# Kernel optimization log

Hardware: AMD Instinct MI355X
Metric: run time of the kernel (lower is better)

The kernel has to match this reference:

```python
import jax, jax.numpy as jnp
import numpy as np

C_CURV = 0.1            # curvature k
SC = float(np.sqrt(C_CURV))
EPS = 1e-7


def _mobius_add(x, y, c):
    x2 = jnp.sum(x * x, -1, keepdims=True)
    y2 = jnp.sum(y * y, -1, keepdims=True)
    xy = jnp.sum(x * y, -1, keepdims=True)
    num = (1 + 2 * c * xy + c * y2) * x + (1 - c * x2) * y
    den = 1 + 2 * c * xy + c * c * x2 * y2
    return num / jnp.maximum(den, 1e-12)


def _mobius_scalarmul(r, x, c):
    sc = jnp.sqrt(c)
    n = jnp.linalg.norm(x, axis=-1, keepdims=True)
    t = jnp.clip(sc * n, EPS, 1.0 - 1e-6)
    return jnp.tanh(r * jnp.arctanh(t)) * x / jnp.maximum(sc * n, EPS)


def setup_inputs() -> dict:
    key = jax.random.key(0)
    k0, k1, k2, k3, k4 = jax.random.split(key, 5)
    B, N, V, D, NC = 64, 1024, 50257, 128, 10
    token_ids = jax.random.randint(k0, (B, N), 0, V)
    mask = jax.random.randint(k1, (B, N), 0, 2).astype(bool)
    emb = (jax.random.normal(k2, (V, D), jnp.float32) * 0.02).at[0].set(0.0)  # pad_id=0 row zeroed
    Wo = jax.random.normal(k3, (D, D + 1), jnp.float32) / np.sqrt(D + 1)
    bo = jnp.zeros((D,), jnp.float32)
    Wf = jax.random.normal(k4, (NC, D), jnp.float32) / np.sqrt(D)
    bf = jnp.zeros((NC,), jnp.float32)
    return {"token_ids": token_ids, "mask": mask, "emb": emb, "Wo": Wo, "bo": bo, "Wf": Wf, "bf": bf}


def reference(token_ids, mask, emb, Wo, bo, Wf, bf):
    c, sc = C_CURV, SC
    D = emb.shape[1]
    # embedding lookup (tangent vectors at origin)
    v = emb[token_ids]                                            # (B,N,D)
    # Lorentz expmap0 -> hyperboloid points in D+1
    nv = jnp.maximum(jnp.linalg.norm(v, axis=-1, keepdims=True), EPS)
    x = jnp.concatenate([jnp.cosh(sc * nv) / sc,
                         jnp.sinh(sc * nv) * v / (sc * nv)], -1)  # (B,N,D+1)
    # single-head attention, scores = -<xi,xj>_L (Lorentz inner), masked softmax
    sgn = jnp.concatenate([-jnp.ones((1,)), jnp.ones((D,))]).astype(x.dtype)
    scores = -jnp.einsum('bid,bjd->bij', x * sgn, x) / np.sqrt(D + 1)
    scores = jnp.where(mask[:, None, :], scores, -1e9)
    w = jax.nn.softmax(scores, axis=-1)
    # riemannian value aggregation: Lorentz centroid (weighted sum renormalized to hyperboloid)
    mu = jnp.einsum('bij,bjd->bid', w, x)
    inner = jnp.einsum('bid,d,bid->bi', mu, sgn, mu)
    mu = mu / (sc * jnp.sqrt(jnp.maximum(-inner, EPS))[..., None])
    # output projection (D+1 -> D) then Poincare expmap0 so points lie in the ball
    u = jnp.einsum('bid,od->bio', mu, Wo) + bo                    # (B,N,D)
    nu = jnp.maximum(jnp.linalg.norm(u, axis=-1, keepdims=True), EPS)
    y = jnp.tanh(sc * nu) * u / (sc * nu)                         # (B,N,D) in ball
    # sequential masked Mobius pooling: left-fold mobius_add over valid tokens, then scalarmul 1/n
    def step(acc, xm):
        xi, mi = xm                                               # (B,D), (B,)
        new = _mobius_add(acc, xi, c)
        return jnp.where(mi[:, None], new, acc), None
    acc0 = jnp.zeros_like(y[:, 0, :])
    acc, _ = jax.lax.scan(step, acc0, (jnp.swapaxes(y, 0, 1), jnp.swapaxes(mask, 0, 1)))
    cnt = jnp.sum(mask, axis=1)
    r = (1.0 / jnp.maximum(cnt, 1))[:, None].astype(y.dtype)
    pooled = _mobius_scalarmul(r, acc, c)
    pooled = jnp.where((cnt > 0)[:, None], pooled, y[:, 0, :])    # empty rows fall back to first token
    # LorentzMLR head: logmap0 then linear
    npn = jnp.maximum(jnp.linalg.norm(pooled, axis=-1, keepdims=True), EPS)
    t = jnp.clip(sc * npn, EPS, 1.0 - 1e-6)
    vlog = jnp.arctanh(t) * pooled / (sc * npn)
    return vlog @ Wf.T + bf                                       # (B, num_classes)
```

## Files before the change

### kernel.cpp

```cpp
#include <hip/hip_runtime.h>
#include <math.h>

#define B_    64
#define N_    1024
#define D_    128
#define DP1   129
#define NC_   10
#define QB    128
#define KT    32
#define SCf   0.31622776601683794f
#define SCALE 0.08804509063256238f

typedef __bf16 bf16x8 __attribute__((ext_vector_type(8)));
typedef float  f32x16 __attribute__((ext_vector_type(16)));
typedef unsigned long long ull;

#define MFMA(a, b, c) __builtin_amdgcn_mfma_f32_32x32x16_bf16((a), (b), (c), 0, 0, 0)

static __device__ __forceinline__ float dpp_add_step(float f, int ctrl, int rmask) {
    if (ctrl == 0x111) { int t = __builtin_amdgcn_update_dpp(0, __builtin_bit_cast(int, f), 0x111, 0xf, 0xf, true); return f + __builtin_bit_cast(float, t); }
    if (ctrl == 0x112) { int t = __builtin_amdgcn_update_dpp(0, __builtin_bit_cast(int, f), 0x112, 0xf, 0xf, true); return f + __builtin_bit_cast(float, t); }
    if (ctrl == 0x114) { int t = __builtin_amdgcn_update_dpp(0, __builtin_bit_cast(int, f), 0x114, 0xf, 0xf, true); return f + __builtin_bit_cast(float, t); }
    if (ctrl == 0x118) { int t = __builtin_amdgcn_update_dpp(0, __builtin_bit_cast(int, f), 0x118, 0xf, 0xf, true); return f + __builtin_bit_cast(float, t); }
    if (ctrl == 0x142 && rmask == 0xa) { int t = __builtin_amdgcn_update_dpp(0, __builtin_bit_cast(int, f), 0x142, 0xa, 0xf, true); return f + __builtin_bit_cast(float, t); }
    { int t = __builtin_amdgcn_update_dpp(0, __builtin_bit_cast(int, f), 0x143, 0xc, 0xf, true); return f + __builtin_bit_cast(float, t); }
}

static __device__ __forceinline__ float wave_sum64(float f) {
    f = dpp_add_step(f, 0x111, 0xf);
    f = dpp_add_step(f, 0x112, 0xf);
    f = dpp_add_step(f, 0x114, 0xf);
    f = dpp_add_step(f, 0x118, 0xf);
    f = dpp_add_step(f, 0x142, 0xa);
    f = dpp_add_step(f, 0x143, 0xc);
    return __builtin_bit_cast(float, __builtin_amdgcn_readlane(__builtin_bit_cast(int, f), 63));
}

static __device__ __forceinline__ float half_sum32(float f, int half) {
    f = dpp_add_step(f, 0x111, 0xf);
    f = dpp_add_step(f, 0x112, 0xf);
    f = dpp_add_step(f, 0x114, 0xf);
    f = dpp_add_step(f, 0x118, 0xf);
    f = dpp_add_step(f, 0x142, 0xa);
    float s0 = __builtin_bit_cast(float, __builtin_amdgcn_readlane(__builtin_bit_cast(int, f), 31));
    float s1 = __builtin_bit_cast(float, __builtin_amdgcn_readlane(__builtin_bit_cast(int, f), 63));
    return half ? s1 : s0;
}

static __device__ __forceinline__ float readlane_f(float v, int lane) {
    return __builtin_bit_cast(float, __builtin_amdgcn_readlane(__builtin_bit_cast(int, v), lane));
}

static __device__ __forceinline__ bf16x8 ld_lds8(const __bf16* p) {
    union { bf16x8 v; ull q[2]; } u;
    u.q[0] = *(const ull*)(p);
    u.q[1] = *(const ull*)(p + 4);
    return u.v;
}

__global__ __launch_bounds__(256) void k_detect_mask(const int* __restrict__ mask_w,
                                                     int* __restrict__ flag) {
    __shared__ int bad;
    if (threadIdx.x == 0) bad = 0;
    __syncthreads();
    int local = 0;
    for (int i = threadIdx.x; i < 16384; i += 256) {
        int v = mask_w[i];
        if (v != 0 && v != 1) local = 1;
    }
    if (local) atomicOr(&bad, 1);
    __syncthreads();
    if (threadIdx.x == 0) *flag = bad;
}

static __device__ __forceinline__ int read_mask(const int* mw, int is_i8, int idx) {
    if (is_i8) return (int)((const unsigned char*)mw)[idx];
    return mw[idx];
}

__global__ __launch_bounds__(256) void k_prep_wo(const float* __restrict__ Wo,
                                                 __bf16* __restrict__ Woh,
                                                 __bf16* __restrict__ Wol) {
    int idx = blockIdx.x * 256 + threadIdx.x;
    if (idx >= 128 * 144) return;
    int o = idx / 144, d = idx - o * 144;
    float v = (d < DP1) ? Wo[o * DP1 + d] : 0.f;
    __bf16 h = (__bf16)v;
    Woh[idx] = h;
    Wol[idx] = (__bf16)(v - (float)h);
}

__global__ __launch_bounds__(256) void k_prep(const int* __restrict__ tok,
                                              const float* __restrict__ emb,
                                              __bf16* __restrict__ Xh, __bf16* __restrict__ Xl,
                                              float* __restrict__ X0g, float* __restrict__ X128g) {
    __shared__ float Xf[64][132];
    const int t = threadIdx.x, w = t >> 6, l = t & 63;
    const int base = blockIdx.x * 64;
    for (int it = 0; it < 16; ++it) {
        const int tk = w * 16 + it;
        const int id = tok[base + tk];
        const float2 v = ((const float2*)(emb + (size_t)id * D_))[l];
        float s = wave_sum64(v.x * v.x + v.y * v.y);
        float nv = fmaxf(sqrtf(s), 1e-7f);
        float a = SCf * nv;
        float a2 = a * a;
        float shc, ch;
        if (a < 0.5f) {
            shc = 1.f + a2 * (1.f/6.f) * (1.f + a2 * (1.f/20.f) * (1.f + a2 * (1.f/42.f)));
            ch  = 1.f + a2 * 0.5f * (1.f + a2 * (1.f/12.f) * (1.f + a2 * (1.f/30.f)));
        } else {
            float ea = __expf(a), ei = 1.f / ea;
            ch = 0.5f * (ea + ei);
            shc = 0.5f * (ea - ei) / a;
        }
        Xf[tk][1 + 2 * l] = v.x * shc;
        Xf[tk][2 + 2 * l] = v.y * shc;
        if (l == 0) Xf[tk][0] = ch / SCf;
    }
    __syncthreads();
    const int tk2 = t >> 2, dg = (t & 3) * 32;
    for (int i = 0; i < 32; i += 8) {
        bf16x8 hv, lv;
        #pragma unroll
        for (int j = 0; j < 8; ++j) {
            float f = Xf[tk2][dg + i + j];
            __bf16 h = (__bf16)f;
            hv[j] = h;
            lv[j] = (__bf16)(f - (float)h);
        }
        *(bf16x8*)(Xh + (size_t)(base + tk2) * D_ + dg + i) = hv;
        *(bf16x8*)(Xl + (size_t)(base + tk2) * D_ + dg + i) = lv;
    }
    if (t < 64) {
        X0g[base + t]   = Xf[t][0];
        X128g[base + t] = Xf[t][D_];
    }
}

__global__ __launch_bounds__(256, 2) void k_attn(
        const __bf16* __restrict__ Xh, const __bf16* __restrict__ Xl,
        const float* __restrict__ X0g, const float* __restrict__ X128g,
        const int* __restrict__ mask, const int* __restrict__ mflag,
        const __bf16* __restrict__ Woh, const __bf16* __restrict__ Wol,
        const float* __restrict__ bo,
        float* __restrict__ Y, float* __restrict__ Y2) {
    extern __shared__ char smem[];
    __bf16* KB = (__bf16*)smem;
    __bf16* Pb = (__bf16*)(smem + 33792);
    __shared__ float K0s[2][KT];
    __shared__ float K128s[2][KT];
    __shared__ int   Ms[2][KT];

    const int b    = blockIdx.x;
    const int qb   = blockIdx.y * QB;
    const int t    = threadIdx.x;
    const int w    = t >> 6;
    const int l    = t & 63;
    const int l31  = l & 31;
    const int half = l >> 5;
    const int is8  = *mflag;

    const size_t qrow = (size_t)(b * N_ + qb + w * 32 + l31);
    bf16x8 qfh[8], qfl[8];
    #pragma unroll
    for (int ks = 0; ks < 8; ++ks) {
        qfh[ks] = *(const bf16x8*)(Xh + qrow * D_ + ks * 16 + half * 8);
        qfl[ks] = *(const bf16x8*)(Xl + qrow * D_ + ks * 16 + half * 8);
    }
    float q0[16], q128[16];
    #pragma unroll
    for (int r = 0; r < 16; ++r) {
        const int qr = (r & 3) + 8 * (r >> 2) + 4 * half;
        q0[r]   = X0g[b * N_ + qb + w * 32 + qr];
        q128[r] = X128g[b * N_ + qb + w * 32 + qr];
    }

    const int skey = t >> 3, sck = t & 7;
    bf16x8 svh0, svh1, svl0, svl1;
    float  sK0 = 0.f, sK128 = 0.f;
    int    sM = 0;
    auto ldg_tile = [&](int kt) {
        const size_t kr = (size_t)(b * N_ + kt * KT + skey);
        svh0 = *(const bf16x8*)(Xh + kr * D_ + sck * 16);
        svh1 = *(const bf16x8*)(Xh + kr * D_ + sck * 16 + 8);
        svl0 = *(const bf16x8*)(Xl + kr * D_ + sck * 16);
        svl1 = *(const bf16x8*)(Xl + kr * D_ + sck * 16 + 8);
        if (t < KT) {
            sK0   = X0g[b * N_ + kt * KT + t];
            sK128 = X128g[b * N_ + kt * KT + t];
            sM    = read_mask(mask, is8, b * N_ + kt * KT + t);
        }
    };
    auto st_tile = [&](int buf) {
        __bf16* KH = KB + buf * 8448;
        __bf16* KL = KH + 4224;
        union { bf16x8 v; ull q[2]; } u;
        u.v = svh0; *(ull*)(KH + skey * 132 + sck * 16)      = u.q[0]; *(ull*)(KH + skey * 132 + sck * 16 + 4)  = u.q[1];
        u.v = svh1; *(ull*)(KH + skey * 132 + sck * 16 + 8)  = u.q[0]; *(ull*)(KH + skey * 132 + sck * 16 + 12) = u.q[1];
        u.v = svl0; *(ull*)(KL + skey * 132 + sck * 16)      = u.q[0]; *(ull*)(KL + skey * 132 + sck * 16 + 4)  = u.q[1];
        u.v = svl1; *(ull*)(KL + skey * 132 + sck * 16 + 8)  = u.q[0]; *(ull*)(KL + skey * 132 + sck * 16 + 12) = u.q[1];
        if (t < KT) { K0s[buf][t] = sK0; K128s[buf][t] = sK128; Ms[buf][t] = sM; }
    };

    f32x16 accM[4] = {};
    float  mu128p[16] = {};

    ldg_tile(0);
    st_tile(0);

    for (int kt = 0; kt < N_ / KT; ++kt) {
        __syncthreads();
        const int cur = kt & 1;
        const int ktn = (kt < 31) ? kt + 1 : 31;
        ldg_tile(ktn);

        const __bf16* KH = KB + cur * 8448;
        const __bf16* KL = KH + 4224;

        f32x16 accS = {};
        #pragma unroll
        for (int ks = 0; ks < 8; ++ks) {
            bf16x8 bh = ld_lds8(KH + l31 * 132 + ks * 16 + half * 8);
            bf16x8 bl = ld_lds8(KL + l31 * 132 + ks * 16 + half * 8);
            accS = MFMA(qfh[ks], bh, accS);
            accS = MFMA(qfh[ks], bl, accS);
            accS = MFMA(qfl[ks], bh, accS);
        }
        const float k0v = K0s[cur][l31], k128v = K128s[cur][l31];
        const int   mv  = Ms[cur][l31];
        #pragma unroll
        for (int r = 0; r < 16; ++r) {
            float sc = (2.f * q0[r] * k0v - accS[r] - q128[r] * k128v) * SCALE;
            float e  = mv ? __expf(sc) : 0.f;
            mu128p[r] += e * k128v;
            __bf16 eh = (__bf16)e;
            __bf16 el = (__bf16)(e - (float)eh);
            const int qr = (r & 3) + 8 * (r >> 2) + 4 * half;
            Pb[(w * 2 + 0) * 1152 + qr * 36 + l31] = eh;
            Pb[(w * 2 + 1) * 1152 + qr * 36 + l31] = el;
        }

        #pragma unroll
        for (int ks = 0; ks < 2; ++ks) {
            bf16x8 ah = ld_lds8(Pb + (w * 2 + 0) * 1152 + l31 * 36 + ks * 16 + half * 8);
            bf16x8 al = ld_lds8(Pb + (w * 2 + 1) * 1152 + l31 * 36 + ks * 16 + half * 8);
            #pragma unroll
            for (int nt = 0; nt < 4; ++nt) {
                const int cmp = nt * 32 + l31;
                bf16x8 bh, bl;
                #pragma unroll
                for (int j = 0; j < 8; ++j) {
                    const int key = ks * 16 + half * 8 + j;
                    bh[j] = KH[key * 132 + cmp];
                    bl[j] = KL[key * 132 + cmp];
                }
                accM[nt] = MFMA(ah, bh, accM[nt]);
                accM[nt] = MFMA(ah, bl, accM[nt]);
                accM[nt] = MFMA(al, bh, accM[nt]);
            }
        }

        st_tile(cur ^ 1);
    }

    #pragma unroll
    for (int r = 0; r < 16; ++r) mu128p[r] = half_sum32(mu128p[r], half);
    float rno[16];
    #pragma unroll
    for (int r = 0; r < 16; ++r) {
        float p = 0.f;
        #pragma unroll
        for (int nt = 0; nt < 4; ++nt) p += accM[nt][r] * accM[nt][r];
        if (l31 == 0) p -= 2.f * accM[0][r] * accM[0][r];
        p = half_sum32(p, half);
        float negI = -(p + mu128p[r] * mu128p[r]);
        negI = fmaxf(negI, 1e-7f);
        rno[r] = 1.f / (SCf * sqrtf(negI));
    }
    #pragma unroll
    for (int nt = 0; nt < 4; ++nt)
        #pragma unroll
        for (int r = 0; r < 16; ++r) accM[nt][r] *= rno[r];
    #pragma unroll
    for (int r = 0; r < 16; ++r) mu128p[r] *= rno[r];

    __syncthreads();
    __bf16* MuA = (__bf16*)smem + w * (32 * 148);
    #pragma unroll
    for (int r = 0; r < 16; ++r) {
        const int qr = (r & 3) + 8 * (r >> 2) + 4 * half;
        #pragma unroll
        for (int nt = 0; nt < 4; ++nt)
            MuA[qr * 148 + nt * 32 + l31] = (__bf16)accM[nt][r];
        if (l31 == 0) MuA[qr * 148 + 128] = (__bf16)mu128p[r];
        if (l31 >= 1 && l31 <= 15) MuA[qr * 148 + 128 + l31] = (__bf16)0.f;
    }
    bf16x8 Ah[9];
    #pragma unroll
    for (int ks = 0; ks < 9; ++ks) Ah[ks] = ld_lds8(MuA + l31 * 148 + ks * 16 + half * 8);
    #pragma unroll
    for (int r = 0; r < 16; ++r) {
        const int qr = (r & 3) + 8 * (r >> 2) + 4 * half;
        #pragma unroll
        for (int nt = 0; nt < 4; ++nt) {
            float m = accM[nt][r];
            MuA[qr * 148 + nt * 32 + l31] = (__bf16)(m - (float)(__bf16)m);
        }
        if (l31 == 0) {
            float m = mu128p[r];
            MuA[qr * 148 + 128] = (__bf16)(m - (float)(__bf16)m);
        }
    }
    bf16x8 Al[9];
    #pragma unroll
    for (int ks = 0; ks < 9; ++ks) Al[ks] = ld_lds8(MuA + l31 * 148 + ks * 16 + half * 8);

    f32x16 accU[4] = {};
    #pragma unroll
    for (int ks = 0; ks < 9; ++ks) {
        #pragma unroll
        for (int nt = 0; nt < 4; ++nt) {
            bf16x8 bh = *(const bf16x8*)(Woh + (size_t)(nt * 32 + l31) * 144 + ks * 16 + half * 8);
            bf16x8 bl = *(const bf16x8*)(Wol + (size_t)(nt * 32 + l31) * 144 + ks * 16 + half * 8);
            accU[nt] = MFMA(Ah[ks], bh, accU[nt]);
            accU[nt] = MFMA(Ah[ks], bl, accU[nt]);
            accU[nt] = MFMA(Al[ks], bh, accU[nt]);
        }
    }

    float bov[4];
    #pragma unroll
    for (int nt = 0; nt < 4; ++nt) bov[nt] = bo[nt * 32 + l31];
    #pragma unroll
    for (int r = 0; r < 16; ++r) {
        float p = 0.f;
        #pragma unroll
        for (int nt = 0; nt < 4; ++nt) {
            float uv = accU[nt][r] + bov[nt];
            accU[nt][r] = uv;
            p += uv * uv;
        }
        float nn = half_sum32(p, half);
        float nu = fmaxf(sqrtf(nn), 1e-7f);
        float aa = SCf * nu;
        float cf = tanhf(aa) / aa;
        const int qr = (r & 3) + 8 * (r >> 2) + 4 * half;
        const size_t row = (size_t)(b * N_ + qb + w * 32 + qr);
        #pragma unroll
        for (int nt = 0; nt < 4; ++nt)
            Y[row * D_ + nt * 32 + l31] = accU[nt][r] * cf;
        if (l31 == 0) Y2[row] = nn * cf * cf;
    }
}

__global__ __launch_bounds__(256) void k_gram(const float* __restrict__ Y,
                                              float* __restrict__ G) {
    const int c = blockIdx.x, b = blockIdx.y;
    const int t = threadIdx.x, w = t >> 6, l = t & 63;
    const int l31 = l & 31, half = l >> 5;
    const int rt = w >> 1, ct = w & 1;
    const size_t base = (size_t)(b * N_ + c * 64);
    const float* Ar = Y + (base + rt * 32 + l31) * D_;
    const float* Br = Y + (base + ct * 32 + l31) * D_;
    f32x16 acc = {};
    #pragma unroll
    for (int ks = 0; ks < 8; ++ks) {
        const int c0 = ks * 16 + half * 8;
        float4 a0 = *(const float4*)(Ar + c0);
        float4 a1 = *(const float4*)(Ar + c0 + 4);
        float4 b0 = *(const float4*)(Br + c0);
        float4 b1 = *(const float4*)(Br + c0 + 4);
        float av[8] = {a0.x, a0.y, a0.z, a0.w, a1.x, a1.y, a1.z, a1.w};
        float bv[8] = {b0.x, b0.y, b0.z, b0.w, b1.x, b1.y, b1.z, b1.w};
        bf16x8 ah, al, bh, bl;
        #pragma unroll
        for (int j = 0; j < 8; ++j) {
            __bf16 h = (__bf16)av[j]; ah[j] = h; al[j] = (__bf16)(av[j] - (float)h);
            __bf16 g = (__bf16)bv[j]; bh[j] = g; bl[j] = (__bf16)(bv[j] - (float)g);
        }
        acc = MFMA(ah, bh, acc);
        acc = MFMA(ah, bl, acc);
        acc = MFMA(al, bh, acc);
    }
    float* Gb = G + ((size_t)(b * 16 + c) << 12);
    #pragma unroll
    for (int r = 0; r < 16; ++r) {
        const int row = rt * 32 + (r & 3) + 8 * (r >> 2) + 4 * half;
        Gb[row * 64 + ct * 32 + l31] = acc[r];
    }
}

__global__ __launch_bounds__(64, 1) void k_pool(const float* __restrict__ Y,
                                                const float* __restrict__ Y2,
                                                const float* __restrict__ G,
                                                const int* __restrict__ mask,
                                                const int* __restrict__ mflag,
                                                const float* __restrict__ Wf,
                                                const float* __restrict__ bf_,
                                                float* __restrict__ out) {
    __shared__ float  prt[64][65];
    __shared__ double vb[D_];
    const int b = blockIdx.x, l = threadIdx.x;
    const int is8 = *mflag;

    int cl = 0;
    for (int i = l; i < N_; i += 64) cl += read_mask(mask, is8, b * N_ + i);
    const int cntT = (int)(wave_sum64((float)cl) + 0.5f);

    const float2* __restrict__ Yp = (const float2*)(Y + (size_t)b * N_ * D_) + l;
    const float*  __restrict__ Gp = G + ((size_t)b << 16) + l;
    const float*  __restrict__ Pp = Y2 + b * N_;

    float  GA[64], GB[64];
    float  py2A, py2B;
    int    msA, msB;
    float2 yring[2][16];

    #pragma unroll
    for (int i = 0; i < 64; ++i) GA[i] = Gp[i * 64];
    py2A = Pp[l];
    msA  = read_mask(mask, is8, b * N_ + l);
    #pragma unroll
    for (int k = 0; k < 16; ++k) yring[0][k] = Yp[(size_t)k * 64];

    float U0 = 0.f, U1 = 0.f, g = 0.f, Dh = 1.f, P = 0.f;

    auto chunk = [&](int c, float (&Gc)[64], float (&Gn)[64],
                     float py2c, float& py2n, int msc, int& msn) {
        const int cn = (c < 15) ? c + 1 : 15;
        #pragma unroll
        for (int i = 0; i < 64; ++i) Gn[i] = Gp[cn * 4096 + i * 64];
        py2n = Pp[cn * 64 + l];
        msn  = read_mask(mask, is8, b * N_ + cn * 64 + l);

        #pragma unroll
        for (int q = 0; q < 4; ++q) {
            #pragma unroll
            for (int k = 0; k < 16; ++k) {
                int gs = c * 64 + (q + 1) * 16 + k;
                if (gs > N_ - 1) gs = N_ - 1;
                yring[(q + 1) & 1][k] = Yp[(size_t)gs * 64];
            }
            #pragma unroll
            for (int k = 0; k < 16; ++k) {
                const int ir = q * 16 + k;
                const float2 yv  = yring[q & 1][k];
                const float  Gv  = Gc[ir];
                const float  py2 = readlane_f(py2c, ir);
                const bool   m   = (__builtin_amdgcn_readlane(msc, ir) != 0);
                const float Dsq   = Dh * Dh;
                const float Bh    = fmaf(-0.1f, P, Dsq);
                const float Donep = Dh * fmaf(0.1f, py2, 1.f);
                const float tP    = (0.01f * py2) * P;
                const float puy  = readlane_f(g, ir);
                const float Ahat = fmaf(0.2f, puy, Donep);
                float dh = fmaf(Dh, fmaf(0.2f, puy, Dh), tP);
                dh = fmaxf(dh, 1e-12f * Dsq);
                const float Draw = m ? dh : Dh;
                const float Am   = m ? Ahat : 1.f;
                const float Bm   = m ? Bh   : 0.f;
                const float Pn   = fmaf(Am, fmaf(Am, P, (2.f * Bm) * puy), (Bm * Bm) * py2);
                if ((k & 3) == 3) {
                    const int e = ilogbf(Draw);
                    const float Aef = ldexpf(Am, -e);
                    const float Bef = ldexpf(Bm, -e);
                    Dh = ldexpf(Draw, -e);
                    P  = ldexpf(Pn, -2 * e);
                    g  = fmaf(Aef, g, Bef * Gv);
                    U0 = fmaf(Aef, U0, Bef * yv.x);
                    U1 = fmaf(Aef, U1, Bef * yv.y);
                } else {
                    Dh = Draw;
                    P  = Pn;
                    g  = fmaf(Am, g, Bm * Gv);
                    U0 = fmaf(Am, U0, Bm * yv.x);
                    U1 = fmaf(Am, U1, Bm * yv.y);
                }
            }
        }
        if (c < 15) {
            const int nb = (c + 1) * 64;
            #pragma unroll
            for (int k0 = 0; k0 < 64; k0 += 16) {
                float2 tmp[16];
                #pragma unroll
                for (int k = 0; k < 16; ++k) tmp[k] = Yp[(size_t)(nb + k0 + k) * 64];
                #pragma unroll
                for (int k = 0; k < 16; ++k)
                    prt[k0 + k][l] = fmaf(U0, tmp[k].x, U1 * tmp[k].y);
            }
            float s0 = 0.f, s1 = 0.f, s2 = 0.f, s3 = 0.f;
            #pragma unroll
            for (int p = 0; p < 64; p += 4) {
                s0 += prt[l][p];     s1 += prt[l][p + 1];
                s2 += prt[l][p + 2]; s3 += prt[l][p + 3];
            }
            g = (s0 + s1) + (s2 + s3);
        }
    };

    for (int cc = 0; cc < 8; ++cc) {
        chunk(2 * cc,     GA, GB, py2A, py2B, msA, msB);
        chunk(2 * cc + 1, GB, GA, py2B, py2A, msB, msA);
    }

    const double SCd = 0.31622776601683794;
    const double sD = 1.0 / (double)Dh;
    double a0 = sD * (double)U0, a1 = sD * (double)U1;
    double n2 = fmax((double)P * (sD * sD), 0.0);
    double n = sqrt(n2);
    double tt = SCd * n;
    tt = fmin(fmax(tt, 1e-7), 1.0 - 1e-6);
    int cm = cntT > 0 ? cntT : 1;
    float rf = (float)(1.0 / (double)cm);
    double r = (double)rf;
    double dv = fmax(SCd * n, 1e-7);
    double f = tanh(r * atanh(tt)) / dv;
    double p0 = a0 * f, p1 = a1 * f;
    double q2;
    if (cntT == 0) {
        float2 y0v = *(const float2*)(Y + (size_t)(b * N_) * D_ + 2 * l);
        p0 = y0v.x; p1 = y0v.y;
        q2 = (double)Y2[b * N_];
    } else {
        q2 = f * f * n2;
    }
    double npn = fmax(sqrt(q2), 1e-7);
    double t2 = fmin(fmax(SCd * npn, 1e-7), 1.0 - 1e-6);
    double f2 = atanh(t2) / (SCd * npn);
    vb[2 * l]     = p0 * f2;
    vb[2 * l + 1] = p1 * f2;
    __syncthreads();

    if (l < NC_) {
        double o = (double)bf_[l];
        for (int d = 0; d < D_; ++d) o += vb[d] * (double)Wf[l * D_ + d];
        out[b * NC_ + l] = (float)o;
    }
}

extern "C" void kernel_launch(void* const* d_in, const int* in_sizes, int n_in,
                              void* d_out, int out_size, void* d_ws, size_t ws_size,
                              hipStream_t stream) {
    const int*   tok  = (const int*)d_in[0];
    const int*   mask = (const int*)d_in[1];
    const float* emb  = (const float*)d_in[2];
    const float* Wo   = (const float*)d_in[3];
    const float* bo   = (const float*)d_in[4];
    const float* Wf   = (const float*)d_in[5];
    const float* bf_  = (const float*)d_in[6];
    float* out = (float*)d_out;

    char* wsb = (char*)d_ws;
    __bf16* Xh   = (__bf16*)wsb;
    __bf16* Xl   = (__bf16*)(wsb + 16777216);
    float*  X0g  = (float*)(wsb + 33554432);
    float*  X128g= (float*)(wsb + 33816576);
    __bf16* Woh  = (__bf16*)(wsb + 34078720);
    __bf16* Wol  = (__bf16*)(wsb + 34115584);
    float*  Y    = (float*)(wsb + 34152448);
    float*  Y2   = (float*)(wsb + 67706880);
    int*    flag = (int*)(wsb + 67969024);
    float*  Gram = (float*)wsb;

    k_detect_mask<<<dim3(1), dim3(256), 0, stream>>>(mask, flag);
    k_prep_wo<<<dim3(72), dim3(256), 0, stream>>>(Wo, Woh, Wol);
    k_prep<<<dim3(B_ * N_ / 64), dim3(256), 0, stream>>>(tok, emb, Xh, Xl, X0g, X128g);
    k_attn<<<dim3(B_, N_ / QB), dim3(256), 53760, stream>>>(Xh, Xl, X0g, X128g, mask, flag,
                                                            Woh, Wol, bo, Y, Y2);
    k_gram<<<dim3(16, B_), dim3(256), 0, stream>>>(Y, Gram);
    k_pool<<<dim3(B_), dim3(64), 0, stream>>>(Y, Y2, Gram, mask, flag, Wf, bf_, out);
}
```

Baseline: 394.6 us.

## Single-buffer K tile in attention kernel to raise occupancy to 4 blocks/CU

Replaces the double-buffered LDS K/mask tile with a single buffer, shrinking dynamic shared memory from 53760 to 37888 bytes, and raises the launch bound to 4 blocks per CU. The store of the next tile now happens at the top of each iteration between two barriers, with the global prefetch issued after the second barrier. The aim is more resident blocks to hide latency. In exchange each iteration gets an extra barrier, and the tighter register budget may cause spills given the large per-thread accumulator and Q fragment state.

```diff
diff --git a/kernel.cpp b/kernel.cpp
--- a/kernel.cpp
+++ b/kernel.cpp
@@ -138,7 +138,7 @@
     }
 }
 
-__global__ __launch_bounds__(256, 2) void k_attn(
+__global__ __launch_bounds__(256, 4) void k_attn(
         const __bf16* __restrict__ Xh, const __bf16* __restrict__ Xl,
         const float* __restrict__ X0g, const float* __restrict__ X128g,
         const int* __restrict__ mask, const int* __restrict__ mflag,
@@ -147,10 +147,10 @@
         float* __restrict__ Y, float* __restrict__ Y2) {
     extern __shared__ char smem[];
     __bf16* KB = (__bf16*)smem;
-    __bf16* Pb = (__bf16*)(smem + 33792);
-    __shared__ float K0s[2][KT];
-    __shared__ float K128s[2][KT];
-    __shared__ int   Ms[2][KT];
+    __bf16* Pb = (__bf16*)(smem + 16896);
+    __shared__ float K0s[KT];
+    __shared__ float K128s[KT];
+    __shared__ int   Ms[KT];
 
     const int b    = blockIdx.x;
     const int qb   = blockIdx.y * QB;
@@ -192,31 +192,30 @@
             sM    = read_mask(mask, is8, b * N_ + kt * KT + t);
         }
     };
-    auto st_tile = [&](int buf) {
-        __bf16* KH = KB + buf * 8448;
-        __bf16* KL = KH + 4224;
+    auto st_tile = [&]() {
+        __bf16* KH = KB;
+        __bf16* KL = KB + 4224;
         union { bf16x8 v; ull q[2]; } u;
         u.v = svh0; *(ull*)(KH + skey * 132 + sck * 16)      = u.q[0]; *(ull*)(KH + skey * 132 + sck * 16 + 4)  = u.q[1];
         u.v = svh1; *(ull*)(KH + skey * 132 + sck * 16 + 8)  = u.q[0]; *(ull*)(KH + skey * 132 + sck * 16 + 12) = u.q[1];
         u.v = svl0; *(ull*)(KL + skey * 132 + sck * 16)      = u.q[0]; *(ull*)(KL + skey * 132 + sck * 16 + 4)  = u.q[1];
         u.v = svl1; *(ull*)(KL + skey * 132 + sck * 16 + 8)  = u.q[0]; *(ull*)(KL + skey * 132 + sck * 16 + 12) = u.q[1];
-        if (t < KT) { K0s[buf][t] = sK0; K128s[buf][t] = sK128; Ms[buf][t] = sM; }
+        if (t < KT) { K0s[t] = sK0; K128s[t] = sK128; Ms[t] = sM; }
     };
 
     f32x16 accM[4] = {};
     float  mu128p[16] = {};
 
     ldg_tile(0);
-    st_tile(0);
 
     for (int kt = 0; kt < N_ / KT; ++kt) {
         __syncthreads();
-        const int cur = kt & 1;
-        const int ktn = (kt < 31) ? kt + 1 : 31;
-        ldg_tile(ktn);
-
-        const __bf16* KH = KB + cur * 8448;
-        const __bf16* KL = KH + 4224;
+        st_tile();
+        __syncthreads();
+        if (kt < 31) ldg_tile(kt + 1);
+
+        const __bf16* KH = KB;
+        const __bf16* KL = KB + 4224;
 
         f32x16 accS = {};
         #pragma unroll
@@ -227,8 +226,8 @@
             accS = MFMA(qfh[ks], bl, accS);
             accS = MFMA(qfl[ks], bh, accS);
         }
-        const float k0v = K0s[cur][l31], k128v = K128s[cur][l31];
-        const int   mv  = Ms[cur][l31];
+        const float k0v = K0s[l31], k128v = K128s[l31];
+        const int   mv  = Ms[l31];
         #pragma unroll
         for (int r = 0; r < 16; ++r) {
             float sc = (2.f * q0[r] * k0v - accS[r] - q128[r] * k128v) * SCALE;
@@ -260,8 +259,6 @@
                 accM[nt] = MFMA(al, bh, accM[nt]);
             }
         }
-
-        st_tile(cur ^ 1);
     }
 
     #pragma unroll
@@ -567,7 +564,7 @@
     k_detect_mask<<<dim3(1), dim3(256), 0, stream>>>(mask, flag);
     k_prep_wo<<<dim3(72), dim3(256), 0, stream>>>(Wo, Woh, Wol);
     k_prep<<<dim3(B_ * N_ / 64), dim3(256), 0, stream>>>(tok, emb, Xh, Xl, X0g, X128g);
-    k_attn<<<dim3(B_, N_ / QB), dim3(256), 53760, stream>>>(Xh, Xl, X0g, X128g, mask, flag,
+    k_attn<<<dim3(B_, N_ / QB), dim3(256), 37888, stream>>>(Xh, Xl, X0g, X128g, mask, flag,
                                                             Woh, Wol, bo, Y, Y2);
     k_gram<<<dim3(16, B_), dim3(256), 0, stream>>>(Y, Gram);
     k_pool<<<dim3(B_), dim3(64), 0, stream>>>(Y, Y2, Gram, mask, flag, Wf, bf_, out);
```

After: 857.3 us. 2.17x slower.
